# Optimization experiments

Hardware: AMD Instinct MI355X
Metric: run time of the kernel (lower is better)

The kernel has to match this reference:

```python
import jax, jax.numpy as jnp
import numpy as np

D = 8  # polynomial degree; with bias present, basis has D columns (P1..PD)


def setup_inputs() -> dict:
    key = jax.random.key(0)
    k1, k2 = jax.random.split(key)
    batch, n_in, n_out = 65536, 256, 64
    x = jax.random.normal(k1, (batch, n_in), dtype=jnp.float32)
    c_basis = jax.random.normal(k2, (n_out, n_in, D), dtype=jnp.float32) * (1.0 / np.sqrt(n_in * D))
    bias = jnp.zeros((n_out,), dtype=jnp.float32)
    return {"x": x, "c_basis": c_basis, "bias": bias}


def _legendre_basis(x):
    # x: (batch, n_in). Returns (batch, n_in, D) = [P1(t), ..., PD(t)], t = tanh(x).
    t = jnp.tanh(x)
    p_prev = jnp.ones_like(t)  # P0
    p_curr = t                 # P1
    polys = [p_curr]
    for k in range(2, D + 1):  # small fixed-length loop over degree
        p_next = ((2 * k - 1) * t * p_curr - (k - 1) * p_prev) / k
        polys.append(p_next)
        p_prev, p_curr = p_curr, p_next
    return jnp.stack(polys, axis=-1)  # (batch, n_in, D)


def reference(x, c_basis, bias):
    # basis: (batch, n_in, D); contract over (n_in, D) with c_basis (n_out, n_in, D)
    leg = _legendre_basis(x)
    y = jnp.einsum('bid,oid->bo', leg, c_basis)
    return y + bias
```

## Files before the change

kernel.cpp:

```cpp
#include <hip/hip_runtime.h>
#include <hip/hip_bf16.h>

typedef _Float16 half2v __attribute__((ext_vector_type(2)));
typedef _Float16 half8 __attribute__((ext_vector_type(8)));
typedef __attribute__((ext_vector_type(4))) float floatx4;
typedef __attribute__((ext_vector_type(4))) unsigned int uintx4;

#define GLOBAL_AS __attribute__((address_space(1)))
#define LDS_AS __attribute__((address_space(3)))

__device__ __forceinline__ void async_ld16(const void* g, void* l) {
  __builtin_amdgcn_global_load_lds((const GLOBAL_AS unsigned int*)g,
                                   (LDS_AS unsigned int*)l, 16, 0, 0);
}

__device__ __forceinline__ half2v h2(float v) {
  return (half2v){(_Float16)v, (_Float16)v};
}

__device__ __forceinline__ void legendre2_f16(float xv0, float xv1,
                                              half8* fa0, half8* fa1) {
  float e0 = __builtin_amdgcn_exp2f(xv0 * 2.885390081777927f);
  float t0 = 1.0f - 2.0f * __builtin_amdgcn_rcpf(e0 + 1.0f);
  float e1 = __builtin_amdgcn_exp2f(xv1 * 2.885390081777927f);
  float t1 = 1.0f - 2.0f * __builtin_amdgcn_rcpf(e1 + 1.0f);
  half2v t;
  { auto tt = __builtin_amdgcn_cvt_pkrtz(t0, t1); __builtin_memcpy(&t, &tt, 4); }
  half2v p1 = t;
  half2v u2 = t * p1, w2 = u2 - h2(1.0f);  half2v p2 = h2(0.5f)      * w2 + u2;
  half2v u3 = t * p2, w3 = u3 - p1;        half2v p3 = h2(2.0f/3.0f) * w3 + u3;
  half2v u4 = t * p3, w4 = u4 - p2;        half2v p4 = h2(0.75f)     * w4 + u4;
  half2v u5 = t * p4, w5 = u5 - p3;        half2v p5 = h2(0.8f)      * w5 + u5;
  half2v u6 = t * p5, w6 = u6 - p4;        half2v p6 = h2(5.0f/6.0f) * w6 + u6;
  half2v u7 = t * p6, w7 = u7 - p5;        half2v p7 = h2(6.0f/7.0f) * w7 + u7;
  half2v u8 = t * p7, w8 = u8 - p6;        half2v p8 = h2(7.0f/8.0f) * w8 + u8;
  unsigned P[8];
  __builtin_memcpy(&P[0], &p1, 4); __builtin_memcpy(&P[1], &p2, 4);
  __builtin_memcpy(&P[2], &p3, 4); __builtin_memcpy(&P[3], &p4, 4);
  __builtin_memcpy(&P[4], &p5, 4); __builtin_memcpy(&P[5], &p6, 4);
  __builtin_memcpy(&P[6], &p7, 4); __builtin_memcpy(&P[7], &p8, 4);
  union { unsigned u[4]; half8 h; } a0, a1;
#pragma unroll
  for (int j = 0; j < 4; ++j) {
    a0.u[j] = __builtin_amdgcn_perm(P[2*j+1], P[2*j], 0x05040100u);
    a1.u[j] = __builtin_amdgcn_perm(P[2*j+1], P[2*j], 0x07060302u);
  }
  *fa0 = a0.h;
  *fa1 = a1.h;
}

__global__ void conv_kernel(const float* __restrict__ cb, _Float16* __restrict__ ws) {
  int t = blockIdx.x * 128 + threadIdx.x;
  int o = t >> 8;
  int i = t & 255;
  const floatx4* s = (const floatx4*)(cb + ((size_t)o * 256 + i) * 8);
  floatx4 v0 = s[0], v1 = s[1];
  union { _Float16 h[8]; uintx4 u; } w;
  w.h[0] = (_Float16)v0.x; w.h[1] = (_Float16)v0.y;
  w.h[2] = (_Float16)v0.z; w.h[3] = (_Float16)v0.w;
  w.h[4] = (_Float16)v1.x; w.h[5] = (_Float16)v1.y;
  w.h[6] = (_Float16)v1.z; w.h[7] = (_Float16)v1.w;
  *(uintx4*)(ws + (size_t)i * 512 + o * 8) = w.u;
}

#define NSTEP 16

__global__ __launch_bounds__(512, 4) void kan_kernel(
    const float* __restrict__ x, const _Float16* __restrict__ ws,
    const float* __restrict__ bias, float* __restrict__ y) {
  __shared__ __align__(16) _Float16 bt[3][8192];
  __shared__ __align__(16) float xs[3][2048];

  const int tid  = threadIdx.x;
  const int wid  = tid >> 6;
  const int kh   = wid >> 2;
  const int rh   = wid & 3;
  const int lane = tid & 63;
  const int m    = lane & 15;
  const int q    = lane >> 4;
  const int rb   = blockIdx.x * 128;

  floatx4 acc[2][4];
#pragma unroll
  for (int a = 0; a < 2; ++a)
#pragma unroll
    for (int nt = 0; nt < 4; ++nt) acc[a][nt] = (floatx4){0.f, 0.f, 0.f, 0.f};

  const _Float16* bsrc0;
  const _Float16* bsrc1;
  {
    int t0 = wid * 2, t1 = wid * 2 + 1;
    bsrc0 = ws + (size_t)((t0 >> 3) * 128 + (t0 & 7)) * 512 + lane * 8;
    bsrc1 = ws + (size_t)((t1 >> 3) * 128 + (t1 & 7)) * 512 + lane * 8;
  }

  const float* xsrc;
  {
    int u = wid * 64 + lane;
    int row = u >> 2;
    int p = (u & 3) ^ ((row >> 1) & 3);
    xsrc = x + (size_t)(rb + row) * 256 + (p >> 1) * 128 + (p & 1) * 4;
  }

  auto stage = [&](int b) {
    async_ld16(bsrc0, &bt[b][(wid * 2 + 0) * 512]);
    async_ld16(bsrc1, &bt[b][(wid * 2 + 1) * 512]);
    bsrc0 += 8 * 512; bsrc1 += 8 * 512;
    async_ld16(xsrc, &xs[b][wid * 256]);
    xsrc += 8;
  };

  stage(0);
  stage(1);

  const int row0 = rh * 32 + m;
  const int sw   = (row0 >> 1) & 3;

  auto compute = [&](int buf) {
#pragma unroll
    for (int ks = 0; ks < 2; ++ks) {
      const int xi = row0 * 16 + (((kh * 2 + ks) ^ sw) << 2) + q;
      float xv0 = xs[buf][xi];
      float xv1 = xs[buf][xi + 256];
      half8 f0, f1;
      legendre2_f16(xv0, xv1, &f0, &f1);
      const _Float16* bp = &bt[buf][(kh * 8 + ks * 4 + q) * 512 + m * 8];
      half8 fb0 = *(const half8*)(bp + 0);
      half8 fb1 = *(const half8*)(bp + 128);
      half8 fb2 = *(const half8*)(bp + 256);
      half8 fb3 = *(const half8*)(bp + 384);
      __builtin_amdgcn_s_setprio(1);
      acc[0][0] = __builtin_amdgcn_mfma_f32_16x16x32_f16(f0, fb0, acc[0][0], 0, 0, 0);
      acc[1][0] = __builtin_amdgcn_mfma_f32_16x16x32_f16(f1, fb0, acc[1][0], 0, 0, 0);
      acc[0][1] = __builtin_amdgcn_mfma_f32_16x16x32_f16(f0, fb1, acc[0][1], 0, 0, 0);
      acc[1][1] = __builtin_amdgcn_mfma_f32_16x16x32_f16(f1, fb1, acc[1][1], 0, 0, 0);
      acc[0][2] = __builtin_amdgcn_mfma_f32_16x16x32_f16(f0, fb2, acc[0][2], 0, 0, 0);
      acc[1][2] = __builtin_amdgcn_mfma_f32_16x16x32_f16(f1, fb2, acc[1][2], 0, 0, 0);
      acc[0][3] = __builtin_amdgcn_mfma_f32_16x16x32_f16(f0, fb3, acc[0][3], 0, 0, 0);
      acc[1][3] = __builtin_amdgcn_mfma_f32_16x16x32_f16(f1, fb3, acc[1][3], 0, 0, 0);
      __builtin_amdgcn_s_setprio(0);
    }
  };

#define STEP(ch, N)                                                            \
  {                                                                            \
    asm volatile("s_barrier" ::: "memory");                                    \
    if constexpr ((ch) + 2 < NSTEP) stage(((ch) + 2) % 3);                     \
    asm volatile("s_waitcnt vmcnt(" #N ")" ::: "memory");                      \
    asm volatile("s_barrier" ::: "memory");                                    \
    compute((ch) % 3);                                                         \
  }

  STEP(0, 6)  STEP(1, 6)  STEP(2, 6)  STEP(3, 6)
  STEP(4, 6)  STEP(5, 6)  STEP(6, 6)  STEP(7, 6)
  STEP(8, 6)  STEP(9, 6)  STEP(10, 6) STEP(11, 6)
  STEP(12, 6) STEP(13, 6) STEP(14, 3) STEP(15, 0)
#undef STEP

  float* red = (float*)&bt[0][0];
  __syncthreads();
  if (kh) {
#pragma unroll
    for (int a = 0; a < 2; ++a)
#pragma unroll
      for (int nt = 0; nt < 4; ++nt)
        *(floatx4*)(red + ((rh * 8 + a * 4 + nt) * 64 + lane) * 4) = acc[a][nt];
  }
  __syncthreads();
  if (!kh) {
    float bv[4];
#pragma unroll
    for (int nt = 0; nt < 4; ++nt) bv[nt] = bias[nt * 16 + m];
#pragma unroll
    for (int a = 0; a < 2; ++a) {
      int gr0 = rb + rh * 32 + a * 16 + q * 4;
#pragma unroll
      for (int nt = 0; nt < 4; ++nt) {
        floatx4 p = *(const floatx4*)(red + ((rh * 8 + a * 4 + nt) * 64 + lane) * 4);
#pragma unroll
        for (int r = 0; r < 4; ++r) {
          y[(size_t)(gr0 + r) * 64 + nt * 16 + m] = acc[a][nt][r] + p[r] + bv[nt];
        }
      }
    }
  }
}

extern "C" void kernel_launch(void* const* d_in, const int* in_sizes, int n_in,
                              void* d_out, int out_size, void* d_ws, size_t ws_size,
                              hipStream_t stream) {
  const float* x    = (const float*)d_in[0];
  const float* cb   = (const float*)d_in[1];
  const float* bias = (const float*)d_in[2];
  float* y = (float*)d_out;
  _Float16* ws = (_Float16*)d_ws;
  int batch = in_sizes[0] / 256;
  hipLaunchKernelGGL(conv_kernel, dim3(128), dim3(128), 0, stream, cb, ws);
  hipLaunchKernelGGL(kan_kernel, dim3(batch / 128), dim3(512), 0, stream, x, ws, bias, y);
}
```

Baseline: 117.6 us.

## Double rows per block and drop intra-block split-K reduction

Each block now covers 256 batch rows instead of 128, with all 8 waves working on distinct 32-row slices across the full K range, rather than two K-halves that are later combined through LDS. The shared-memory reduction and its two __syncthreads are removed, and each B tile loaded into LDS is reused by twice as many rows. The cost is a larger x staging buffer, four k-steps per stage instead of two, a lower occupancy hint, and half as many blocks, which may reduce latency hiding.

```diff
diff --git a/kernel.cpp b/kernel.cpp
--- a/kernel.cpp
+++ b/kernel.cpp
@@ -65,20 +65,18 @@
 
 #define NSTEP 16
 
-__global__ __launch_bounds__(512, 4) void kan_kernel(
+__global__ __launch_bounds__(512, 2) void kan_kernel(
     const float* __restrict__ x, const _Float16* __restrict__ ws,
     const float* __restrict__ bias, float* __restrict__ y) {
   __shared__ __align__(16) _Float16 bt[3][8192];
-  __shared__ __align__(16) float xs[3][2048];
+  __shared__ __align__(16) float xs[3][4096];
 
   const int tid  = threadIdx.x;
   const int wid  = tid >> 6;
-  const int kh   = wid >> 2;
-  const int rh   = wid & 3;
   const int lane = tid & 63;
   const int m    = lane & 15;
   const int q    = lane >> 4;
-  const int rb   = blockIdx.x * 128;
+  const int rb   = blockIdx.x * 256;
 
   floatx4 acc[2][4];
 #pragma unroll
@@ -86,45 +84,44 @@
 #pragma unroll
     for (int nt = 0; nt < 4; ++nt) acc[a][nt] = (floatx4){0.f, 0.f, 0.f, 0.f};
 
-  const _Float16* bsrc0;
-  const _Float16* bsrc1;
+  const _Float16* bsrc0 = ws + (size_t)(wid * 2 + 0) * 512 + lane * 8;
+  const _Float16* bsrc1 = ws + (size_t)(wid * 2 + 1) * 512 + lane * 8;
+
+  const float* xsrc0;
+  const float* xsrc1;
   {
-    int t0 = wid * 2, t1 = wid * 2 + 1;
-    bsrc0 = ws + (size_t)((t0 >> 3) * 128 + (t0 & 7)) * 512 + lane * 8;
-    bsrc1 = ws + (size_t)((t1 >> 3) * 128 + (t1 & 7)) * 512 + lane * 8;
-  }
-
-  const float* xsrc;
-  {
-    int u = wid * 64 + lane;
-    int row = u >> 2;
-    int p = (u & 3) ^ ((row >> 1) & 3);
-    xsrc = x + (size_t)(rb + row) * 256 + (p >> 1) * 128 + (p & 1) * 4;
+    int u0 = wid * 128 + lane;
+    int r0_ = u0 >> 2, p0 = (u0 & 3) ^ ((r0_ >> 1) & 3);
+    xsrc0 = x + (size_t)(rb + r0_) * 256 + p0 * 4;
+    int u1 = wid * 128 + 64 + lane;
+    int r1_ = u1 >> 2, p1 = (u1 & 3) ^ ((r1_ >> 1) & 3);
+    xsrc1 = x + (size_t)(rb + r1_) * 256 + p1 * 4;
   }
 
   auto stage = [&](int b) {
     async_ld16(bsrc0, &bt[b][(wid * 2 + 0) * 512]);
     async_ld16(bsrc1, &bt[b][(wid * 2 + 1) * 512]);
-    bsrc0 += 8 * 512; bsrc1 += 8 * 512;
-    async_ld16(xsrc, &xs[b][wid * 256]);
-    xsrc += 8;
+    bsrc0 += 8192; bsrc1 += 8192;
+    async_ld16(xsrc0, &xs[b][wid * 512]);
+    async_ld16(xsrc1, &xs[b][wid * 512 + 256]);
+    xsrc0 += 16; xsrc1 += 16;
   };
 
   stage(0);
   stage(1);
 
-  const int row0 = rh * 32 + m;
-  const int sw   = (row0 >> 1) & 3;
+  const int row0 = wid * 32 + m;
+  const int sw   = (m >> 1) & 3;
 
   auto compute = [&](int buf) {
 #pragma unroll
-    for (int ks = 0; ks < 2; ++ks) {
-      const int xi = row0 * 16 + (((kh * 2 + ks) ^ sw) << 2) + q;
+    for (int ks = 0; ks < 4; ++ks) {
+      const int xi = row0 * 16 + ((ks ^ sw) << 2) + q;
       float xv0 = xs[buf][xi];
       float xv1 = xs[buf][xi + 256];
       half8 f0, f1;
       legendre2_f16(xv0, xv1, &f0, &f1);
-      const _Float16* bp = &bt[buf][(kh * 8 + ks * 4 + q) * 512 + m * 8];
+      const _Float16* bp = &bt[buf][(ks * 4 + q) * 512 + m * 8];
       half8 fb0 = *(const half8*)(bp + 0);
       half8 fb1 = *(const half8*)(bp + 128);
       half8 fb2 = *(const half8*)(bp + 256);
@@ -151,36 +148,23 @@
     compute((ch) % 3);                                                         \
   }
 
-  STEP(0, 6)  STEP(1, 6)  STEP(2, 6)  STEP(3, 6)
-  STEP(4, 6)  STEP(5, 6)  STEP(6, 6)  STEP(7, 6)
-  STEP(8, 6)  STEP(9, 6)  STEP(10, 6) STEP(11, 6)
-  STEP(12, 6) STEP(13, 6) STEP(14, 3) STEP(15, 0)
+  STEP(0, 8)  STEP(1, 8)  STEP(2, 8)  STEP(3, 8)
+  STEP(4, 8)  STEP(5, 8)  STEP(6, 8)  STEP(7, 8)
+  STEP(8, 8)  STEP(9, 8)  STEP(10, 8) STEP(11, 8)
+  STEP(12, 8) STEP(13, 8) STEP(14, 4) STEP(15, 0)
 #undef STEP
 
-  float* red = (float*)&bt[0][0];
-  __syncthreads();
-  if (kh) {
+  float bv[4];
 #pragma unroll
-    for (int a = 0; a < 2; ++a)
+  for (int nt = 0; nt < 4; ++nt) bv[nt] = bias[nt * 16 + m];
 #pragma unroll
-      for (int nt = 0; nt < 4; ++nt)
-        *(floatx4*)(red + ((rh * 8 + a * 4 + nt) * 64 + lane) * 4) = acc[a][nt];
-  }
-  __syncthreads();
-  if (!kh) {
-    float bv[4];
+  for (int a = 0; a < 2; ++a) {
+    int gr0 = rb + wid * 32 + a * 16 + q * 4;
 #pragma unroll
-    for (int nt = 0; nt < 4; ++nt) bv[nt] = bias[nt * 16 + m];
+    for (int nt = 0; nt < 4; ++nt) {
 #pragma unroll
-    for (int a = 0; a < 2; ++a) {
-      int gr0 = rb + rh * 32 + a * 16 + q * 4;
-#pragma unroll
-      for (int nt = 0; nt < 4; ++nt) {
-        floatx4 p = *(const floatx4*)(red + ((rh * 8 + a * 4 + nt) * 64 + lane) * 4);
-#pragma unroll
-        for (int r = 0; r < 4; ++r) {
-          y[(size_t)(gr0 + r) * 64 + nt * 16 + m] = acc[a][nt][r] + p[r] + bv[nt];
-        }
+      for (int r = 0; r < 4; ++r) {
+        y[(size_t)(gr0 + r) * 64 + nt * 16 + m] = acc[a][nt][r] + bv[nt];
       }
     }
   }
@@ -196,5 +180,5 @@
   _Float16* ws = (_Float16*)d_ws;
   int batch = in_sizes[0] / 256;
   hipLaunchKernelGGL(conv_kernel, dim3(128), dim3(128), 0, stream, cb, ws);
-  hipLaunchKernelGGL(kan_kernel, dim3(batch / 128), dim3(512), 0, stream, x, ws, bias, y);
+  hipLaunchKernelGGL(kan_kernel, dim3(batch / 256), dim3(512), 0, stream, x, ws, bias, y);
 }
```

Result: no change. 118.9 us (+1.1%).
